# Kernel optimization log

Hardware: AMD Instinct MI355X
Metric: run time of the kernel (lower is better)

## Reference

```python
import jax, jax.numpy as jnp
import numpy as np

E = 8           # moe_num_experts
H = 1024        # hidden_size
F = 4096        # ffn_hidden_size per expert
DL = 256        # d_low (AoE low-dim activation)
TPE = 1024      # tokens per expert (capacity-balanced topology)


def setup_inputs() -> dict:
    key = jax.random.key(0)
    k = jax.random.split(key, 5)
    x = jax.random.normal(k[0], (E * TPE, H), dtype=jnp.float32)
    acts = jax.random.normal(k[1], (E * TPE, DL), dtype=jnp.float32)
    # expert weights, row-major stacked per expert as in create_dmoe_expert_weights
    wup = jax.random.normal(k[2], (E, F, DL), dtype=jnp.float32) * 0.02
    v1 = jax.random.normal(k[3], (E, F, H), dtype=jnp.float32) * 0.02
    w2 = jax.random.normal(k[4], (E, F, H), dtype=jnp.float32) * 0.02
    return {"x": x, "acts": acts, "wup": wup, "v1": v1, "w2": w2,
            "tokens_per_expert": TPE}


def reference(x, acts, wup, v1, w2, tokens_per_expert):
    # Tokens are pre-sorted/grouped by expert (the `topo` block-sparse
    # topology with equal, capacity-balanced groups). The stk sdd/mul/dsd
    # pipeline is then exactly a grouped GLU FFN per expert.
    e = wup.shape[0]
    xg = x.reshape(e, tokens_per_expert, x.shape[-1])        # [E, T, H]
    ag = acts.reshape(e, tokens_per_expert, acts.shape[-1])  # [E, T, DL]
    x1 = jnp.einsum('etl,efl->etf', ag, wup)   # sdd(acts, wup.t(), topo)
    x2 = jnp.einsum('eth,efh->etf', xg, v1)    # sdd(x, v1.t(), topo)
    h = jax.nn.silu(x1) * x2                   # act_fn + stk.ops.mul
    out = jnp.einsum('etf,efh->eth', h, w2)    # dsd(x1, w2)
    return out.reshape(x.shape)
```

## Files before the change

kernel.cpp:

```cpp
#include <hip/hip_runtime.h>

#define E_   8
#define H_   1024
#define F_   4096
#define DL_  256
#define TPE_ 1024
#define TT_  (E_ * TPE_)

typedef __attribute__((ext_vector_type(8))) short  short8;
typedef __attribute__((ext_vector_type(4))) float  f32x4;

__device__ __forceinline__ unsigned short f2bf(float f) {
  unsigned int u = __float_as_uint(f);
  u += 0x7fffu + ((u >> 16) & 1u);
  return (unsigned short)(u >> 16);
}

__device__ __forceinline__ void glds16(const void* g, void* l) {
  __builtin_amdgcn_global_load_lds(
      (const __attribute__((address_space(1))) unsigned int*)g,
      (__attribute__((address_space(3))) unsigned int*)l, 16, 0, 0);
}

__global__ void conv_bf16(const float* __restrict__ src,
                          unsigned short* __restrict__ dst, int n4) {
  int i = blockIdx.x * blockDim.x + threadIdx.x;
  int stride = gridDim.x * blockDim.x;
  for (; i < n4; i += stride) {
    float4 v = ((const float4*)src)[i];
    ushort4 o;
    o.x = f2bf(v.x); o.y = f2bf(v.y); o.z = f2bf(v.z); o.w = f2bf(v.w);
    ((ushort4*)dst)[i] = o;
  }
}

__global__ void transpose_conv(const float* __restrict__ src,
                               unsigned short* __restrict__ dst) {
  __shared__ unsigned short tile[64][65];
  const int e  = blockIdx.z;
  const int f0 = blockIdx.x * 64;
  const int h0 = blockIdx.y * 64;
  const float* s = src + (size_t)e * F_ * H_ + (size_t)f0 * H_ + h0;
#pragma unroll
  for (int it = 0; it < 16; ++it) {
    int lin = it * 256 + threadIdx.x;
    int r = lin >> 6, c = lin & 63;
    tile[r][c] = f2bf(s[(size_t)r * H_ + c]);
  }
  __syncthreads();
  unsigned short* d = dst + (size_t)e * H_ * F_ + (size_t)h0 * F_ + f0;
#pragma unroll
  for (int it = 0; it < 16; ++it) {
    int lin = it * 256 + threadIdx.x;
    int a = lin >> 6, b = lin & 63;
    d[(size_t)a * F_ + b] = tile[b][a];
  }
}

__device__ __forceinline__ void stage_tile(const unsigned short* __restrict__ g,
                                           int ld, unsigned short* lds,
                                           int wid, int lane) {
#pragma unroll
  for (int q = 0; q < 4; ++q) {
    int row = wid * 32 + q * 8 + (lane >> 3);
    int col = (lane & 7) << 3;
    glds16(g + (size_t)row * ld + col, lds + (size_t)(wid * 32 + q * 8) * 64);
  }
}

#define KSTEP(ACC)                                                             \
  __syncthreads();                                                             \
  _Pragma("unroll")                                                            \
  for (int kk = 0; kk < 2; ++kk) {                                             \
    short8 af[4], bfr[4];                                                      \
    _Pragma("unroll")                                                          \
    for (int i = 0; i < 4; ++i)                                                \
      af[i] = *(const short8*)&As[(size_t)(wr * 64 + i * 16 + (lane & 15)) * 64 \
                                  + kk * 32 + (lane >> 4) * 8];                \
    _Pragma("unroll")                                                          \
    for (int j = 0; j < 4; ++j)                                                \
      bfr[j] = *(const short8*)&Bs[(size_t)(wc * 64 + j * 16 + (lane & 15)) * 64 \
                                   + kk * 32 + (lane >> 4) * 8];               \
    _Pragma("unroll")                                                          \
    for (int i = 0; i < 4; ++i)                                                \
      _Pragma("unroll")                                                        \
      for (int j = 0; j < 4; ++j)                                              \
        ACC[i][j] = __builtin_amdgcn_mfma_f32_16x16x32_bf16(af[i], bfr[j],     \
                                                            ACC[i][j], 0, 0, 0); \
  }                                                                            \
  __syncthreads();

__global__ void __launch_bounds__(256, 2)
gemm1_kernel(const unsigned short* __restrict__ ab,
             const unsigned short* __restrict__ xb,
             const unsigned short* __restrict__ wupb,
             const unsigned short* __restrict__ v1b,
             unsigned short* __restrict__ hb) {
  __shared__ __align__(16) unsigned short As[128 * 64];
  __shared__ __align__(16) unsigned short Bs[128 * 64];
  const int bid = blockIdx.x;
  const int e  = bid >> 8;
  const int rr = bid & 255;
  const int mt = rr >> 5;
  const int nt = rr & 31;
  const int m0 = e * TPE_ + mt * 128;
  const int n0 = nt * 128;
  const int lane = threadIdx.x & 63;
  const int wid  = threadIdx.x >> 6;
  const int wr = wid >> 1, wc = wid & 1;

  f32x4 acc1[4][4], acc2[4][4];
#pragma unroll
  for (int i = 0; i < 4; ++i)
#pragma unroll
    for (int j = 0; j < 4; ++j) { acc1[i][j] = (f32x4)0.0f; acc2[i][j] = (f32x4)0.0f; }

  {
    const unsigned short* Ab = ab + (size_t)m0 * DL_;
    const unsigned short* Bb = wupb + (size_t)e * F_ * DL_ + (size_t)n0 * DL_;
    for (int kt = 0; kt < DL_ / 64; ++kt) {
      stage_tile(Ab + kt * 64, DL_, As, wid, lane);
      stage_tile(Bb + kt * 64, DL_, Bs, wid, lane);
      KSTEP(acc1)
    }
  }
  {
    const unsigned short* Ab = xb + (size_t)m0 * H_;
    const unsigned short* Bb = v1b + (size_t)e * F_ * H_ + (size_t)n0 * H_;
    for (int kt = 0; kt < H_ / 64; ++kt) {
      stage_tile(Ab + kt * 64, H_, As, wid, lane);
      stage_tile(Bb + kt * 64, H_, Bs, wid, lane);
      KSTEP(acc2)
    }
  }
#pragma unroll
  for (int i = 0; i < 4; ++i)
#pragma unroll
    for (int j = 0; j < 4; ++j)
#pragma unroll
      for (int r = 0; r < 4; ++r) {
        int row = m0 + wr * 64 + i * 16 + (lane >> 4) * 4 + r;
        int col = n0 + wc * 64 + j * 16 + (lane & 15);
        float g = acc1[i][j][r];
        float u = acc2[i][j][r];
        float s = g / (1.0f + __expf(-g));
        hb[(size_t)row * F_ + col] = f2bf(s * u);
      }
}

__global__ void __launch_bounds__(256, 2)
gemm2_kernel(const unsigned short* __restrict__ hb,
             const unsigned short* __restrict__ w2tb,
             float* __restrict__ out) {
  __shared__ __align__(16) unsigned short As[128 * 64];
  __shared__ __align__(16) unsigned short Bs[128 * 64];
  const int bid = blockIdx.x;
  const int e  = bid >> 6;
  const int rr = bid & 63;
  const int mt = rr >> 3;
  const int nt = rr & 7;
  const int m0 = e * TPE_ + mt * 128;
  const int n0 = nt * 128;
  const int lane = threadIdx.x & 63;
  const int wid  = threadIdx.x >> 6;
  const int wr = wid >> 1, wc = wid & 1;

  f32x4 acc[4][4];
#pragma unroll
  for (int i = 0; i < 4; ++i)
#pragma unroll
    for (int j = 0; j < 4; ++j) acc[i][j] = (f32x4)0.0f;

  const unsigned short* Ab = hb + (size_t)m0 * F_;
  const unsigned short* Bb = w2tb + (size_t)e * H_ * F_ + (size_t)n0 * F_;
  for (int kt = 0; kt < F_ / 64; ++kt) {
    stage_tile(Ab + kt * 64, F_, As, wid, lane);
    stage_tile(Bb + kt * 64, F_, Bs, wid, lane);
    KSTEP(acc)
  }
#pragma unroll
  for (int i = 0; i < 4; ++i)
#pragma unroll
    for (int j = 0; j < 4; ++j)
#pragma unroll
      for (int r = 0; r < 4; ++r) {
        int row = m0 + wr * 64 + i * 16 + (lane >> 4) * 4 + r;
        int col = n0 + wc * 64 + j * 16 + (lane & 15);
        out[(size_t)row * H_ + col] = acc[i][j][r];
      }
}

extern "C" void kernel_launch(void* const* d_in, const int* in_sizes, int n_in,
                              void* d_out, int out_size, void* d_ws, size_t ws_size,
                              hipStream_t stream) {
  const float* x    = (const float*)d_in[0];
  const float* acts = (const float*)d_in[1];
  const float* wup  = (const float*)d_in[2];
  const float* v1   = (const float*)d_in[3];
  const float* w2   = (const float*)d_in[4];
  float* out = (float*)d_out;

  unsigned short* ws   = (unsigned short*)d_ws;
  unsigned short* hb   = ws;
  unsigned short* xb   = hb   + (size_t)TT_ * F_;
  unsigned short* abuf = xb   + (size_t)TT_ * H_;
  unsigned short* wupb = abuf + (size_t)TT_ * DL_;
  unsigned short* v1b  = wupb + (size_t)E_ * F_ * DL_;
  unsigned short* w2tb = v1b  + (size_t)E_ * F_ * H_;

  conv_bf16<<<2048, 256, 0, stream>>>(x,    xb,   (TT_ * H_) / 4);
  conv_bf16<<<1024, 256, 0, stream>>>(acts, abuf, (TT_ * DL_) / 4);
  conv_bf16<<<2048, 256, 0, stream>>>(wup,  wupb, (E_ * F_ * DL_) / 4);
  conv_bf16<<<2048, 256, 0, stream>>>(v1,   v1b,  (E_ * F_ * H_) / 4);
  transpose_conv<<<dim3(F_ / 64, H_ / 64, E_), 256, 0, stream>>>(w2, w2tb);

  gemm1_kernel<<<E_ * (TPE_ / 128) * (F_ / 128), 256, 0, stream>>>(
      abuf, xb, wupb, v1b, hb);
  gemm2_kernel<<<E_ * (TPE_ / 128) * (H_ / 128), 256, 0, stream>>>(
      hb, w2tb, out);
}
```

Measured before the change: 613.9 us.

## Merge conversion kernels into one prep launch and split gate GEMM out

Folds the four bf16 conversion launches and the w2 transpose into a single prep kernel. The transpose now uses float4 loads and short8 stores. The fused gemm1 is split into two kernels: one computes silu(acts·wup) and writes it to hb in bf16, and a second computes x·v1 and multiplies it into hb in place. The split drops the dual accumulator set, which is meant to lower register pressure and raise occupancy. The cost is an extra round trip of the 64MB bf16 hb buffer and a second rounding of the gate value.

New measurement: 596.5 us. 1.03x faster.

```diff
diff --git a/kernel.cpp b/kernel.cpp
--- a/kernel.cpp
+++ b/kernel.cpp
@@ -15,6 +15,9 @@
   u += 0x7fffu + ((u >> 16) & 1u);
   return (unsigned short)(u >> 16);
 }
+__device__ __forceinline__ float bf2f(unsigned short b) {
+  return __uint_as_float(((unsigned int)b) << 16);
+}
 
 __device__ __forceinline__ void glds16(const void* g, void* l) {
   __builtin_amdgcn_global_load_lds(
@@ -22,38 +25,66 @@
       (__attribute__((address_space(3))) unsigned int*)l, 16, 0, 0);
 }
 
-__global__ void conv_bf16(const float* __restrict__ src,
-                          unsigned short* __restrict__ dst, int n4) {
-  int i = blockIdx.x * blockDim.x + threadIdx.x;
-  int stride = gridDim.x * blockDim.x;
-  for (; i < n4; i += stride) {
-    float4 v = ((const float4*)src)[i];
-    ushort4 o;
-    o.x = f2bf(v.x); o.y = f2bf(v.y); o.z = f2bf(v.z); o.w = f2bf(v.w);
-    ((ushort4*)dst)[i] = o;
-  }
-}
-
-__global__ void transpose_conv(const float* __restrict__ src,
-                               unsigned short* __restrict__ dst) {
-  __shared__ unsigned short tile[64][65];
-  const int e  = blockIdx.z;
-  const int f0 = blockIdx.x * 64;
-  const int h0 = blockIdx.y * 64;
-  const float* s = src + (size_t)e * F_ * H_ + (size_t)f0 * H_ + h0;
-#pragma unroll
-  for (int it = 0; it < 16; ++it) {
-    int lin = it * 256 + threadIdx.x;
-    int r = lin >> 6, c = lin & 63;
-    tile[r][c] = f2bf(s[(size_t)r * H_ + c]);
-  }
-  __syncthreads();
-  unsigned short* d = dst + (size_t)e * H_ * F_ + (size_t)h0 * F_ + f0;
-#pragma unroll
-  for (int it = 0; it < 16; ++it) {
-    int lin = it * 256 + threadIdx.x;
-    int a = lin >> 6, b = lin & 63;
-    d[(size_t)a * F_ + b] = tile[b][a];
+#define NCONV_ 2048
+__global__ void prep_kernel(const float* __restrict__ x,
+                            const float* __restrict__ acts,
+                            const float* __restrict__ wup,
+                            const float* __restrict__ v1,
+                            const float* __restrict__ w2,
+                            unsigned short* __restrict__ xb,
+                            unsigned short* __restrict__ ab,
+                            unsigned short* __restrict__ wupb,
+                            unsigned short* __restrict__ v1b,
+                            unsigned short* __restrict__ w2tb) {
+  __shared__ __align__(16) unsigned short tileT[64][72];
+  if (blockIdx.x < NCONV_) {
+    const int c0 = (TT_ * H_) / 4;
+    const int c1 = c0 + (TT_ * DL_) / 4;
+    const int c2 = c1 + (E_ * F_ * DL_) / 4;
+    const int c3 = c2 + (E_ * F_ * H_) / 4;
+    int i = blockIdx.x * blockDim.x + threadIdx.x;
+    const int stride = NCONV_ * 256;
+    for (; i < c3; i += stride) {
+      const float4* s;
+      ushort4* d;
+      int j;
+      if (i < c0)      { s = (const float4*)x   + i;        d = (ushort4*)xb   + i; }
+      else if (i < c1) { j = i - c0; s = (const float4*)acts + j; d = (ushort4*)ab   + j; }
+      else if (i < c2) { j = i - c1; s = (const float4*)wup  + j; d = (ushort4*)wupb + j; }
+      else             { j = i - c2; s = (const float4*)v1   + j; d = (ushort4*)v1b  + j; }
+      float4 v = *s;
+      ushort4 o;
+      o.x = f2bf(v.x); o.y = f2bf(v.y); o.z = f2bf(v.z); o.w = f2bf(v.w);
+      *d = o;
+    }
+  } else {
+    const int t  = blockIdx.x - NCONV_;
+    const int e  = t >> 10;
+    const int r  = t & 1023;
+    const int fb = r >> 4;
+    const int hbk = r & 15;
+    const int tid = threadIdx.x;
+    const float* s = w2 + (size_t)e * F_ * H_ + (size_t)fb * 64 * H_ + hbk * 64;
+#pragma unroll
+    for (int it = 0; it < 4; ++it) {
+      int lin = it * 256 + tid;
+      int f  = lin >> 4;
+      int h4 = (lin & 15) << 2;
+      float4 v = *(const float4*)(s + (size_t)f * H_ + h4);
+      tileT[h4 + 0][f] = f2bf(v.x);
+      tileT[h4 + 1][f] = f2bf(v.y);
+      tileT[h4 + 2][f] = f2bf(v.z);
+      tileT[h4 + 3][f] = f2bf(v.w);
+    }
+    __syncthreads();
+    unsigned short* d = w2tb + (size_t)e * H_ * F_ + (size_t)(hbk * 64) * F_ + fb * 64;
+#pragma unroll
+    for (int it = 0; it < 2; ++it) {
+      int lin = it * 256 + tid;
+      int h  = lin >> 3;
+      int f8 = (lin & 7) << 3;
+      *(short8*)(d + (size_t)h * F_ + f8) = *(const short8*)&tileT[h][f8];
+    }
   }
 }
 
@@ -90,48 +121,36 @@
   }                                                                            \
   __syncthreads();
 
+#define TILE_PROLOGUE(NT_PER_E)                                                \
+  __shared__ __align__(16) unsigned short As[128 * 64];                        \
+  __shared__ __align__(16) unsigned short Bs[128 * 64];                        \
+  const int bid = blockIdx.x;                                                  \
+  const int e   = bid / (8 * NT_PER_E);                                        \
+  const int rr  = bid % (8 * NT_PER_E);                                        \
+  const int mt  = rr / NT_PER_E;                                               \
+  const int nt  = rr % NT_PER_E;                                               \
+  const int m0  = e * TPE_ + mt * 128;                                         \
+  const int n0  = nt * 128;                                                    \
+  const int lane = threadIdx.x & 63;                                           \
+  const int wid  = threadIdx.x >> 6;                                           \
+  const int wr = wid >> 1, wc = wid & 1;                                       \
+  f32x4 acc[4][4];                                                             \
+  _Pragma("unroll")                                                            \
+  for (int i = 0; i < 4; ++i)                                                  \
+    _Pragma("unroll")                                                          \
+    for (int j = 0; j < 4; ++j) acc[i][j] = (f32x4)0.0f;
+
 __global__ void __launch_bounds__(256, 2)
-gemm1_kernel(const unsigned short* __restrict__ ab,
-             const unsigned short* __restrict__ xb,
-             const unsigned short* __restrict__ wupb,
-             const unsigned short* __restrict__ v1b,
-             unsigned short* __restrict__ hb) {
-  __shared__ __align__(16) unsigned short As[128 * 64];
-  __shared__ __align__(16) unsigned short Bs[128 * 64];
-  const int bid = blockIdx.x;
-  const int e  = bid >> 8;
-  const int rr = bid & 255;
-  const int mt = rr >> 5;
-  const int nt = rr & 31;
-  const int m0 = e * TPE_ + mt * 128;
-  const int n0 = nt * 128;
-  const int lane = threadIdx.x & 63;
-  const int wid  = threadIdx.x >> 6;
-  const int wr = wid >> 1, wc = wid & 1;
-
-  f32x4 acc1[4][4], acc2[4][4];
-#pragma unroll
-  for (int i = 0; i < 4; ++i)
-#pragma unroll
-    for (int j = 0; j < 4; ++j) { acc1[i][j] = (f32x4)0.0f; acc2[i][j] = (f32x4)0.0f; }
-
-  {
-    const unsigned short* Ab = ab + (size_t)m0 * DL_;
-    const unsigned short* Bb = wupb + (size_t)e * F_ * DL_ + (size_t)n0 * DL_;
-    for (int kt = 0; kt < DL_ / 64; ++kt) {
-      stage_tile(Ab + kt * 64, DL_, As, wid, lane);
-      stage_tile(Bb + kt * 64, DL_, Bs, wid, lane);
-      KSTEP(acc1)
-    }
-  }
-  {
-    const unsigned short* Ab = xb + (size_t)m0 * H_;
-    const unsigned short* Bb = v1b + (size_t)e * F_ * H_ + (size_t)n0 * H_;
-    for (int kt = 0; kt < H_ / 64; ++kt) {
-      stage_tile(Ab + kt * 64, H_, As, wid, lane);
-      stage_tile(Bb + kt * 64, H_, Bs, wid, lane);
-      KSTEP(acc2)
-    }
+gemm_x1_kernel(const unsigned short* __restrict__ ab,
+               const unsigned short* __restrict__ wupb,
+               unsigned short* __restrict__ gb) {
+  TILE_PROLOGUE(32)
+  const unsigned short* Ab = ab + (size_t)m0 * DL_;
+  const unsigned short* Bb = wupb + (size_t)e * F_ * DL_ + (size_t)n0 * DL_;
+  for (int kt = 0; kt < DL_ / 64; ++kt) {
+    stage_tile(Ab + kt * 64, DL_, As, wid, lane);
+    stage_tile(Bb + kt * 64, DL_, Bs, wid, lane);
+    KSTEP(acc)
   }
 #pragma unroll
   for (int i = 0; i < 4; ++i)
@@ -141,10 +160,35 @@
       for (int r = 0; r < 4; ++r) {
         int row = m0 + wr * 64 + i * 16 + (lane >> 4) * 4 + r;
         int col = n0 + wc * 64 + j * 16 + (lane & 15);
-        float g = acc1[i][j][r];
-        float u = acc2[i][j][r];
+        float g = acc[i][j][r];
         float s = g / (1.0f + __expf(-g));
-        hb[(size_t)row * F_ + col] = f2bf(s * u);
+        gb[(size_t)row * F_ + col] = f2bf(s);
+      }
+}
+
+__global__ void __launch_bounds__(256, 2)
+gemm_h_kernel(const unsigned short* __restrict__ xb,
+              const unsigned short* __restrict__ v1b,
+              unsigned short* __restrict__ hb) {
+  TILE_PROLOGUE(32)
+  const unsigned short* Ab = xb + (size_t)m0 * H_;
+  const unsigned short* Bb = v1b + (size_t)e * F_ * H_ + (size_t)n0 * H_;
+  for (int kt = 0; kt < H_ / 64; ++kt) {
+    stage_tile(Ab + kt * 64, H_, As, wid, lane);
+    stage_tile(Bb + kt * 64, H_, Bs, wid, lane);
+    KSTEP(acc)
+  }
+#pragma unroll
+  for (int i = 0; i < 4; ++i)
+#pragma unroll
+    for (int j = 0; j < 4; ++j)
+#pragma unroll
+      for (int r = 0; r < 4; ++r) {
+        int row = m0 + wr * 64 + i * 16 + (lane >> 4) * 4 + r;
+        int col = n0 + wc * 64 + j * 16 + (lane & 15);
+        size_t idx = (size_t)row * F_ + col;
+        float h = bf2f(hb[idx]) * acc[i][j][r];
+        hb[idx] = f2bf(h);
       }
 }
 
@@ -152,25 +196,7 @@
 gemm2_kernel(const unsigned short* __restrict__ hb,
              const unsigned short* __restrict__ w2tb,
              float* __restrict__ out) {
-  __shared__ __align__(16) unsigned short As[128 * 64];
-  __shared__ __align__(16) unsigned short Bs[128 * 64];
-  const int bid = blockIdx.x;
-  const int e  = bid >> 6;
-  const int rr = bid & 63;
-  const int mt = rr >> 3;
-  const int nt = rr & 7;
-  const int m0 = e * TPE_ + mt * 128;
-  const int n0 = nt * 128;
-  const int lane = threadIdx.x & 63;
-  const int wid  = threadIdx.x >> 6;
-  const int wr = wid >> 1, wc = wid & 1;
-
-  f32x4 acc[4][4];
-#pragma unroll
-  for (int i = 0; i < 4; ++i)
-#pragma unroll
-    for (int j = 0; j < 4; ++j) acc[i][j] = (f32x4)0.0f;
-
+  TILE_PROLOGUE(8)
   const unsigned short* Ab = hb + (size_t)m0 * F_;
   const unsigned short* Bb = w2tb + (size_t)e * H_ * F_ + (size_t)n0 * F_;
   for (int kt = 0; kt < F_ / 64; ++kt) {
@@ -208,14 +234,9 @@
   unsigned short* v1b  = wupb + (size_t)E_ * F_ * DL_;
   unsigned short* w2tb = v1b  + (size_t)E_ * F_ * H_;
 
-  conv_bf16<<<2048, 256, 0, stream>>>(x,    xb,   (TT_ * H_) / 4);
-  conv_bf16<<<1024, 256, 0, stream>>>(acts, abuf, (TT_ * DL_) / 4);
-  conv_bf16<<<2048, 256, 0, stream>>>(wup,  wupb, (E_ * F_ * DL_) / 4);
-  conv_bf16<<<2048, 256, 0, stream>>>(v1,   v1b,  (E_ * F_ * H_) / 4);
-  transpose_conv<<<dim3(F_ / 64, H_ / 64, E_), 256, 0, stream>>>(w2, w2tb);
-
-  gemm1_kernel<<<E_ * (TPE_ / 128) * (F_ / 128), 256, 0, stream>>>(
-      abuf, xb, wupb, v1b, hb);
-  gemm2_kernel<<<E_ * (TPE_ / 128) * (H_ / 128), 256, 0, stream>>>(
-      hb, w2tb, out);
-}
+  prep_kernel<<<NCONV_ + (F_ / 64) * (H_ / 64) * E_, 256, 0, stream>>>(
+      x, acts, wup, v1, w2, xb, abuf, wupb, v1b, w2tb);
+  gemm_x1_kernel<<<E_ * 8 * 32, 256, 0, stream>>>(abuf, wupb, hb);
+  gemm_h_kernel<<<E_ * 8 * 32, 256, 0, stream>>>(xb, v1b, hb);
+  gemm2_kernel<<<E_ * 8 * 8, 256, 0, stream>>>(hb, w2tb, out);
+}
```
